# Optimization experiments

Hardware: AMD Instinct MI355X
Metric: run time of the kernel (lower is better)

The kernel has to match this reference:

```python
import jax, jax.numpy as jnp
import numpy as np

N, E, D = 100000, 1000000, 128  # nodes, edges, feature/embedding dim


def setup_inputs() -> dict:
    key = jax.random.key(0)
    ks = jax.random.split(key, 8)
    s = 1.0 / np.sqrt(D)
    return {
        "x": jax.random.normal(ks[0], (N, D), jnp.float32),
        "edge_index": jax.random.randint(ks[1], (2, E), 0, N, jnp.int32),
        # layer 1: lin_l (with bias) on aggregated neighbors, lin_r (no bias) on root
        "W1_l": jax.random.normal(ks[2], (D, D), jnp.float32) * s,
        "b1_l": jnp.zeros((D,), jnp.float32),
        "W1_r": jax.random.normal(ks[3], (D, D), jnp.float32) * s,
        # layer 2
        "W2_l": jax.random.normal(ks[4], (D, D), jnp.float32) * s,
        "b2_l": jnp.zeros((D,), jnp.float32),
        "W2_r": jax.random.normal(ks[5], (D, D), jnp.float32) * s,
    }


def _sage_conv(x, src, dst, Wl, bl, Wr):
    # PyG SAGEConv (aggr='mean'): out = lin_l(mean_{j->i} x_j) + lin_r(x_i)
    msgs = x[src]                                            # [E, D] gather
    agg = jax.ops.segment_sum(msgs, dst, num_segments=N)     # [N, D] scatter-add
    cnt = jax.ops.segment_sum(jnp.ones((src.shape[0],), x.dtype), dst,
                              num_segments=N)                # [N]
    mean = agg / jnp.maximum(cnt, 1.0)[:, None]
    return mean @ Wl + bl + x @ Wr


def reference(x, edge_index, W1_l, b1_l, W1_r, W2_l, b2_l, W2_r):
    src, dst = edge_index[0], edge_index[1]
    h = jax.nn.relu(_sage_conv(x, src, dst, W1_l, b1_l, W1_r))  # dropout inactive (eval)
    return _sage_conv(h, src, dst, W2_l, b2_l, W2_r)            # [N, D] embeddings
```

## Files before the change

kernel.cpp:

```cpp
#include <hip/hip_runtime.h>

#define D 128
constexpr int NPB   = 128;
constexpr int BCAP  = 1536;
constexpr int SEGB  = 8192;
constexpr int KMAX  = 1024;

typedef __bf16 bf16x8 __attribute__((ext_vector_type(8)));
typedef float f32x4 __attribute__((ext_vector_type(4)));
typedef int intv4 __attribute__((ext_vector_type(4)));

__device__ __forceinline__ unsigned short f2bf(float f) {
    unsigned int u = __float_as_uint(f);
    unsigned int r = (u + 0x7fffu + ((u >> 16) & 1u)) >> 16;
    return (unsigned short)r;
}
__device__ __forceinline__ unsigned pack2(float a, float b) {
    return (unsigned)f2bf(a) | ((unsigned)f2bf(b) << 16);
}
__device__ __forceinline__ int q8clamp(float v) {
    int q = __float2int_rn(v);
    return min(max(q, -127), 127);
}

__global__ __launch_bounds__(256) void front_kernel(
    const int* __restrict__ src, const int* __restrict__ dst,
    unsigned long long* __restrict__ bucket, int* __restrict__ bCur,
    int E, int K, int NB,
    const float* __restrict__ W1l, const float* __restrict__ W1r,
    const float* __restrict__ W2l, const float* __restrict__ W2r,
    unsigned short* __restrict__ Wpack,
    const float* __restrict__ xin, unsigned short* __restrict__ xb,
    unsigned* __restrict__ xq, float* __restrict__ sx, int n4)
{
    const int t = threadIdx.x;
    if (blockIdx.x < (unsigned)NB) {
        __shared__ int lcnt[KMAX], lbase[KMAX];
        for (int i = t; i < K; i += 256) lcnt[i] = 0;
        __syncthreads();

        const int base = blockIdx.x * SEGB;
        intv4 dreg[8], sreg[8];
#pragma unroll
        for (int c = 0; c < 4; ++c) {
            int e0 = base + c * 2048 + t * 8;
            if (e0 + 8 <= E) {
                dreg[2*c]   = __builtin_nontemporal_load(reinterpret_cast<const intv4*>(dst + e0));
                dreg[2*c+1] = __builtin_nontemporal_load(reinterpret_cast<const intv4*>(dst + e0 + 4));
                sreg[2*c]   = __builtin_nontemporal_load(reinterpret_cast<const intv4*>(src + e0));
                sreg[2*c+1] = __builtin_nontemporal_load(reinterpret_cast<const intv4*>(src + e0 + 4));
            } else {
#pragma unroll
                for (int k = 0; k < 4; ++k) {
                    dreg[2*c][k]   = (e0 + k < E) ? dst[e0 + k] : -1;
                    dreg[2*c+1][k] = (e0 + 4 + k < E) ? dst[e0 + 4 + k] : -1;
                    sreg[2*c][k]   = (e0 + k < E) ? src[e0 + k] : 0;
                    sreg[2*c+1][k] = (e0 + 4 + k < E) ? src[e0 + 4 + k] : 0;
                }
            }
#pragma unroll
            for (int k = 0; k < 8; ++k) {
                int d = dreg[2*c + (k >> 2)][k & 3];
                if (d >= 0) atomicAdd(&lcnt[d >> 7], 1);
            }
        }
        __syncthreads();
        for (int i = t; i < K; i += 256) {
            int c = lcnt[i];
            lbase[i] = c ? atomicAdd(&bCur[i], c) : 0;
            lcnt[i] = 0;
        }
        __syncthreads();
#pragma unroll
        for (int c = 0; c < 4; ++c) {
#pragma unroll
            for (int k = 0; k < 8; ++k) {
                int d = dreg[2*c + (k >> 2)][k & 3];
                int s = sreg[2*c + (k >> 2)][k & 3];
                if (d >= 0) {
                    int b = d >> 7;
                    int p = lbase[b] + atomicAdd(&lcnt[b], 1);
                    if (p < BCAP)
                        bucket[(size_t)b * BCAP + p] =
                            ((unsigned long long)(unsigned)s << 32) | (unsigned)d;
                }
            }
        }
    } else if (blockIdx.x < (unsigned)(NB + 32)) {
        int b = (blockIdx.x - NB) * 4 + (t >> 6);
        int l = t & 63;
        int layer = b >> 6, wsel = (b >> 5) & 1, kt = (b >> 3) & 3, ct = b & 7;
        const float* W = layer ? (wsel ? W2r : W2l) : (wsel ? W1r : W1l);
        int k0  = kt * 32 + (l >> 4) * 8;
        int col = ct * 16 + (l & 15);
        unsigned short tmp[8];
#pragma unroll
        for (int j = 0; j < 8; ++j) tmp[j] = f2bf(W[(k0 + j) * D + col]);
        size_t fbase = (((size_t)layer * 64 + wsel * 32 + kt * 8 + ct) * 64 + l) * 8;
        uint4 o;
        o.x = (unsigned)tmp[0] | ((unsigned)tmp[1] << 16);
        o.y = (unsigned)tmp[2] | ((unsigned)tmp[3] << 16);
        o.z = (unsigned)tmp[4] | ((unsigned)tmp[5] << 16);
        o.w = (unsigned)tmp[6] | ((unsigned)tmp[7] << 16);
        *reinterpret_cast<uint4*>(Wpack + fbase) = o;
    } else {
        int i = (blockIdx.x - NB - 32) * 256 + t;
        if (i < n4) {
            float4 v = reinterpret_cast<const float4*>(xin)[i];
            ushort4 o;
            o.x = f2bf(v.x); o.y = f2bf(v.y); o.z = f2bf(v.z); o.w = f2bf(v.w);
            reinterpret_cast<ushort4*>(xb)[i] = o;
            float am = fmaxf(fmaxf(fabsf(v.x), fabsf(v.y)),
                             fmaxf(fabsf(v.z), fabsf(v.w)));
#pragma unroll
            for (int off = 1; off < 32; off <<= 1)
                am = fmaxf(am, __shfl_xor(am, off, 32));
            am = fmaxf(am, 1e-20f);
            float inv = 127.0f / am;
            unsigned q = ((unsigned)(q8clamp(v.x * inv) & 0xff))
                       | ((unsigned)(q8clamp(v.y * inv) & 0xff) << 8)
                       | ((unsigned)(q8clamp(v.z * inv) & 0xff) << 16)
                       | ((unsigned)(q8clamp(v.w * inv) & 0xff) << 24);
            xq[i] = q;
            if ((t & 31) == 0) sx[i >> 5] = am / 127.0f;
        }
    }
}

__global__ __launch_bounds__(256) void csrbuild_kernel(
    const unsigned long long* __restrict__ bucket, const int* __restrict__ bCur,
    int2* __restrict__ offe, int* __restrict__ csr, int K, int N)
{
    __shared__ unsigned long long ebuf[BCAP];
    __shared__ int lhist[NPB], sc[NPB], lcur[NPB];
    __shared__ int red[256];
    const int t = threadIdx.x;
    const int b = blockIdx.x;

    int s = 0;
    for (int i = t; i < b; i += 256) s += bCur[i];
    red[t] = s;
    __syncthreads();
    for (int o = 128; o; o >>= 1) {
        if (t < o) red[t] += red[t + o];
        __syncthreads();
    }
    const int gbase = red[0];
    const int cnt = min(bCur[b], BCAP);

    if (t < NPB) lhist[t] = 0;
    __syncthreads();

    const unsigned long long* bp = bucket + (size_t)b * BCAP;
    for (int i = t; i < cnt; i += 256) {
        unsigned long long e = bp[i];
        ebuf[i] = e;
        atomicAdd(&lhist[(int)(e & 127ULL)], 1);
    }
    __syncthreads();

    if (t < NPB) sc[t] = lhist[t];
    __syncthreads();
    for (int o = 1; o < NPB; o <<= 1) {
        int y = 0;
        if (t < NPB && t >= o) y = sc[t - o];
        __syncthreads();
        if (t < NPB) sc[t] += y;
        __syncthreads();
    }
    if (t < NPB) {
        int node = b * NPB + t;
        int excl = sc[t] - lhist[t];
        lcur[t] = excl;
        if (node < N) offe[node] = make_int2(gbase + excl, gbase + sc[t]);
    }
    __syncthreads();

    for (int i = t; i < cnt; i += 256) {
        unsigned long long e = ebuf[i];
        int dl = (int)(e & 127ULL);
        int p = gbase + atomicAdd(&lcur[dl], 1);
        csr[p] = (int)(e >> 32);
    }
}

__device__ __forceinline__ void acc8(uint2 v, float sc, float* acc) {
#pragma unroll
    for (int w = 0; w < 2; ++w) {
        unsigned x = w ? v.y : v.x;
#pragma unroll
        for (int b = 0; b < 4; ++b) {
            int e = (int)((signed char)((x >> (8 * b)) & 0xffu));
            acc[4 * w + b] = fmaf((float)e, sc, acc[4 * w + b]);
        }
    }
}

__global__ __launch_bounds__(256) void gather8_i8(
    const uint2* __restrict__ q8, const float* __restrict__ scales,
    const int2* __restrict__ offe, const int* __restrict__ csr,
    unsigned short* __restrict__ mean, int N)
{
    int tid = blockIdx.x * 256 + threadIdx.x;
    int n   = tid >> 4;
    int q   = tid & 15;
    if (n >= N) return;
    int2 be = offe[n];
    int b = be.x, e = be.y;
    const uint2* fp = q8 + q;

    float acc[8];
#pragma unroll
    for (int i = 0; i < 8; ++i) acc[i] = 0.f;

    int j = b;
    for (; j + 3 < e; j += 4) {
        int s0 = __builtin_nontemporal_load(csr + j);
        int s1 = __builtin_nontemporal_load(csr + j + 1);
        int s2 = __builtin_nontemporal_load(csr + j + 2);
        int s3 = __builtin_nontemporal_load(csr + j + 3);
        uint2 v0 = fp[(size_t)s0 * 16];
        uint2 v1 = fp[(size_t)s1 * 16];
        uint2 v2 = fp[(size_t)s2 * 16];
        uint2 v3 = fp[(size_t)s3 * 16];
        float c0 = scales[s0];
        float c1 = scales[s1];
        float c2 = scales[s2];
        float c3 = scales[s3];
        acc8(v0, c0, acc);
        acc8(v1, c1, acc);
        acc8(v2, c2, acc);
        acc8(v3, c3, acc);
    }
    for (; j < e; ++j) {
        int s0 = csr[j];
        uint2 v0 = fp[(size_t)s0 * 16];
        acc8(v0, scales[s0], acc);
    }
    float invd = 1.0f / (float)max(e - b, 1);
#pragma unroll
    for (int i = 0; i < 8; ++i) acc[i] *= invd;
    uint4 o;
    o.x = pack2(acc[0], acc[1]);
    o.y = pack2(acc[2], acc[3]);
    o.z = pack2(acc[4], acc[5]);
    o.w = pack2(acc[6], acc[7]);
    *reinterpret_cast<uint4*>(mean + (size_t)n * D + q * 8) = o;
}

template <int RELU, int OUT_BF16, int QUANT>
__global__ __launch_bounds__(256, 2) void sage_mfma(
    const unsigned short* __restrict__ meanb,
    const unsigned short* __restrict__ xb,
    const unsigned short* __restrict__ Wpack,
    const float* __restrict__ bl,
    void* __restrict__ outv,
    signed char* __restrict__ hq, float* __restrict__ sh,
    int Mtiles, int TPB)
{
    __shared__ __align__(16) char sbuf[2][8192];
    __shared__ int rowmaxI[16];
    const int t    = threadIdx.x;
    const int lane = t & 63;
    const int wc   = t >> 6;
    const int l15  = lane & 15;
    const int lhi  = lane >> 4;

    bf16x8 bfrag[2][8];
#pragma unroll
    for (int ktt = 0; ktt < 8; ++ktt) {
        int wsel = ktt >> 2, kt = ktt & 3;
#pragma unroll
        for (int c = 0; c < 2; ++c) {
            int ct = wc * 2 + c;
            size_t fbase = ((size_t)(wsel * 32 + kt * 8 + ct) * 64 + lane) * 8;
            bfrag[c][ktt] = *reinterpret_cast<const bf16x8*>(Wpack + fbase);
        }
    }
    float bias[2];
    bias[0] = bl[wc * 32 + l15];
    bias[1] = bl[wc * 32 + 16 + l15];

    int tile0 = blockIdx.x * TPB;
    if (tile0 >= Mtiles) return;
    int tend = min(tile0 + TPB, Mtiles);

    const int sr = t >> 4;
    const int sq = t & 15;
    const int ss = sq ^ (sr & 7);
    char* dstM = &sbuf[0][sr * 256 + ss * 16];
    char* dstX = &sbuf[0][4096 + sr * 256 + ss * 16];

    {
        size_t gofs = (size_t)(tile0 * 16 + sr) * D + sq * 8;
        *reinterpret_cast<uint4*>(dstM) = *reinterpret_cast<const uint4*>(meanb + gofs);
        *reinterpret_cast<uint4*>(dstX) = *reinterpret_cast<const uint4*>(xb + gofs);
    }
    int cur = 0;

    for (int it = tile0; it < tend; ++it) {
        __syncthreads();
        const bool pf = (it + 1 < tend);
        uint4 mv, xv;
        if (pf) {
            size_t gofs = (size_t)((it + 1) * 16 + sr) * D + sq * 8;
            mv = *reinterpret_cast<const uint4*>(meanb + gofs);
            xv = *reinterpret_cast<const uint4*>(xb + gofs);
        }

        f32x4 acc0 = {0.f, 0.f, 0.f, 0.f};
        f32x4 acc1 = {0.f, 0.f, 0.f, 0.f};
        const char* base = sbuf[cur];
#pragma unroll
        for (int ktt = 0; ktt < 8; ++ktt) {
            int p = ktt >> 2, kt = ktt & 3;
            int q = kt * 4 + lhi;
            int byteoff = p * 4096 + l15 * 256 + ((q ^ (l15 & 7)) * 16);
            bf16x8 a = *reinterpret_cast<const bf16x8*>(base + byteoff);
            acc0 = __builtin_amdgcn_mfma_f32_16x16x32_bf16(a, bfrag[0][ktt], acc0, 0, 0, 0);
            acc1 = __builtin_amdgcn_mfma_f32_16x16x32_bf16(a, bfrag[1][ktt], acc1, 0, 0, 0);
        }

        int rbase = it * 16 + lhi * 4;
        float v[2][4];
#pragma unroll
        for (int c = 0; c < 2; ++c) {
            const f32x4& a = c ? acc1 : acc0;
#pragma unroll
            for (int r = 0; r < 4; ++r) {
                float w = a[r] + bias[c];
                if (RELU) w = fmaxf(w, 0.f);
                v[c][r] = w;
            }
        }
#pragma unroll
        for (int c = 0; c < 2; ++c) {
            int col = wc * 32 + c * 16 + l15;
#pragma unroll
            for (int r = 0; r < 4; ++r) {
                if (OUT_BF16) {
                    ((unsigned short*)outv)[(size_t)(rbase + r) * D + col] = f2bf(v[c][r]);
                } else {
                    ((float*)outv)[(size_t)(rbase + r) * D + col] = v[c][r];
                }
            }
        }

        if (QUANT) {
            float m[4];
#pragma unroll
            for (int r = 0; r < 4; ++r) m[r] = fmaxf(v[0][r], v[1][r]);
#pragma unroll
            for (int mask = 1; mask < 16; mask <<= 1)
#pragma unroll
                for (int r = 0; r < 4; ++r)
                    m[r] = fmaxf(m[r], __shfl_xor(m[r], mask, 64));
            __syncthreads();
            if (t < 16) rowmaxI[t] = 0;
            __syncthreads();
            if (l15 == 0) {
#pragma unroll
                for (int r = 0; r < 4; ++r)
                    atomicMax(&rowmaxI[lhi * 4 + r], __float_as_int(m[r]));
            }
            __syncthreads();
#pragma unroll
            for (int r = 0; r < 4; ++r) {
                float rm = __int_as_float(rowmaxI[lhi * 4 + r]);
                float inv = 127.0f / fmaxf(rm, 1e-20f);
                int row = rbase + r;
#pragma unroll
                for (int c = 0; c < 2; ++c) {
                    int col = wc * 32 + c * 16 + l15;
                    hq[(size_t)row * D + col] = (signed char)q8clamp(v[c][r] * inv);
                }
                if (wc == 0 && l15 == 0) sh[row] = rm / 127.0f;
            }
        }

        if (pf) {
            char* dM = dstM + (cur ^ 1) * 8192;
            char* dX = dstX + (cur ^ 1) * 8192;
            *reinterpret_cast<uint4*>(dM) = mv;
            *reinterpret_cast<uint4*>(dX) = xv;
            cur ^= 1;
        }
    }
}

extern "C" void kernel_launch(void* const* d_in, const int* in_sizes, int n_in,
                              void* d_out, int out_size, void* d_ws, size_t ws_size,
                              hipStream_t stream) {
    const float* x   = (const float*)d_in[0];
    const int*   ei  = (const int*)d_in[1];
    const float* W1l = (const float*)d_in[2];
    const float* b1l = (const float*)d_in[3];
    const float* W1r = (const float*)d_in[4];
    const float* W2l = (const float*)d_in[5];
    const float* b2l = (const float*)d_in[6];
    const float* W2r = (const float*)d_in[7];
    float* out = (float*)d_out;

    const int N = in_sizes[0] / D;
    const int E = in_sizes[1] / 2;
    const int* src = ei;
    const int* dst = ei + E;

    const int K = (N + NPB - 1) / NPB;

    unsigned short* xb    = (unsigned short*)d_ws;
    unsigned short* meanb = xb + (size_t)N * D;
    unsigned short* hb    = meanb + (size_t)N * D;
    unsigned short* Wpack = hb + (size_t)N * D;
    int* bCur     = (int*)(Wpack + 65536);
    int2* offe    = (int2*)(bCur + KMAX);
    int* csr_src  = (int*)(offe + N);
    float* sx     = (float*)(csr_src + E);
    float* sh     = sx + N;
    signed char* hq = (signed char*)(sh + N);

    unsigned long long* bucket = (unsigned long long*)hb;
    unsigned* xq = (unsigned*)((char*)hb + (size_t)K * BCAP * 8);

    const int Mtiles  = (N + 15) / 16;
    const int TPB     = 8;
    const int gemmGrid = (Mtiles + TPB - 1) / TPB;
    const int gatherBlocks = (int)(((long long)N * 16 + 255) / 256);
    const int NB = (E + SEGB - 1) / SEGB;
    const int n4 = N * D / 4;
    const int convBlocks = (n4 + 255) / 256;

    hipMemsetAsync(bCur, 0, (size_t)K * sizeof(int), stream);
    front_kernel<<<NB + 32 + convBlocks, 256, 0, stream>>>(
        src, dst, bucket, bCur, E, K, NB,
        W1l, W1r, W2l, W2r, Wpack, x, xb, xq, sx, n4);
    csrbuild_kernel<<<K, 256, 0, stream>>>(bucket, bCur, offe, csr_src, K, N);

    gather8_i8<<<gatherBlocks, 256, 0, stream>>>(
        (const uint2*)xq, sx, offe, csr_src, meanb, N);
    sage_mfma<1, 1, 1><<<gemmGrid, 256, 0, stream>>>(
        meanb, xb, Wpack, b1l, hb, hq, sh, Mtiles, TPB);

    gather8_i8<<<gatherBlocks, 256, 0, stream>>>(
        (const uint2*)hq, sh, offe, csr_src, meanb, N);
    sage_mfma<0, 0, 0><<<gemmGrid, 256, 0, stream>>>(
        meanb, hb, Wpack + 32768, b2l, out, nullptr, nullptr, Mtiles, TPB);
}
```

Before: 149.8 us.

## Fuse neighbor mean-gather into the MFMA SAGE layer kernel

Replaces the separate int8 gather kernel and the bf16 MFMA GEMM kernel with one kernel per layer. Each block gathers and averages neighbor features for its 16-row tile directly into LDS, then runs the MFMA GEMM on that tile. This removes the write and re-read of the intermediate mean buffer and one launch per layer. In exchange it drops the double-buffered prefetch, exposes gather latency between barriers, lowers tiles per block and adds a 3-blocks-per-CU launch bound that may limit occupancy for the latency-bound gather. The quantized input buffer is moved into the now-unused mean workspace so it does not overlap the hidden-layer output written in the same kernel.

```diff
diff --git a/kernel.cpp b/kernel.cpp
--- a/kernel.cpp
+++ b/kernel.cpp
@@ -196,69 +196,18 @@
     }
 }
 
-__global__ __launch_bounds__(256) void gather8_i8(
+template <int RELU, int OUT_BF16, int QUANT>
+__global__ __launch_bounds__(256, 3) void sage_fused(
     const uint2* __restrict__ q8, const float* __restrict__ scales,
     const int2* __restrict__ offe, const int* __restrict__ csr,
-    unsigned short* __restrict__ mean, int N)
-{
-    int tid = blockIdx.x * 256 + threadIdx.x;
-    int n   = tid >> 4;
-    int q   = tid & 15;
-    if (n >= N) return;
-    int2 be = offe[n];
-    int b = be.x, e = be.y;
-    const uint2* fp = q8 + q;
-
-    float acc[8];
-#pragma unroll
-    for (int i = 0; i < 8; ++i) acc[i] = 0.f;
-
-    int j = b;
-    for (; j + 3 < e; j += 4) {
-        int s0 = __builtin_nontemporal_load(csr + j);
-        int s1 = __builtin_nontemporal_load(csr + j + 1);
-        int s2 = __builtin_nontemporal_load(csr + j + 2);
-        int s3 = __builtin_nontemporal_load(csr + j + 3);
-        uint2 v0 = fp[(size_t)s0 * 16];
-        uint2 v1 = fp[(size_t)s1 * 16];
-        uint2 v2 = fp[(size_t)s2 * 16];
-        uint2 v3 = fp[(size_t)s3 * 16];
-        float c0 = scales[s0];
-        float c1 = scales[s1];
-        float c2 = scales[s2];
-        float c3 = scales[s3];
-        acc8(v0, c0, acc);
-        acc8(v1, c1, acc);
-        acc8(v2, c2, acc);
-        acc8(v3, c3, acc);
-    }
-    for (; j < e; ++j) {
-        int s0 = csr[j];
-        uint2 v0 = fp[(size_t)s0 * 16];
-        acc8(v0, scales[s0], acc);
-    }
-    float invd = 1.0f / (float)max(e - b, 1);
-#pragma unroll
-    for (int i = 0; i < 8; ++i) acc[i] *= invd;
-    uint4 o;
-    o.x = pack2(acc[0], acc[1]);
-    o.y = pack2(acc[2], acc[3]);
-    o.z = pack2(acc[4], acc[5]);
-    o.w = pack2(acc[6], acc[7]);
-    *reinterpret_cast<uint4*>(mean + (size_t)n * D + q * 8) = o;
-}
-
-template <int RELU, int OUT_BF16, int QUANT>
-__global__ __launch_bounds__(256, 2) void sage_mfma(
-    const unsigned short* __restrict__ meanb,
-    const unsigned short* __restrict__ xb,
+    const unsigned short* __restrict__ xside,
     const unsigned short* __restrict__ Wpack,
     const float* __restrict__ bl,
     void* __restrict__ outv,
     signed char* __restrict__ hq, float* __restrict__ sh,
-    int Mtiles, int TPB)
+    int Mtiles, int TPB, int N)
 {
-    __shared__ __align__(16) char sbuf[2][8192];
+    __shared__ __align__(16) char sbuf[8192];
     __shared__ int rowmaxI[16];
     const int t    = threadIdx.x;
     const int lane = t & 63;
@@ -288,35 +237,69 @@
     const int sr = t >> 4;
     const int sq = t & 15;
     const int ss = sq ^ (sr & 7);
-    char* dstM = &sbuf[0][sr * 256 + ss * 16];
-    char* dstX = &sbuf[0][4096 + sr * 256 + ss * 16];
-
-    {
-        size_t gofs = (size_t)(tile0 * 16 + sr) * D + sq * 8;
-        *reinterpret_cast<uint4*>(dstM) = *reinterpret_cast<const uint4*>(meanb + gofs);
-        *reinterpret_cast<uint4*>(dstX) = *reinterpret_cast<const uint4*>(xb + gofs);
-    }
-    int cur = 0;
+    char* dstM = &sbuf[sr * 256 + ss * 16];
+    char* dstX = &sbuf[4096 + sr * 256 + ss * 16];
+    const uint2* fp = q8 + sq;
 
     for (int it = tile0; it < tend; ++it) {
-        __syncthreads();
-        const bool pf = (it + 1 < tend);
-        uint4 mv, xv;
-        if (pf) {
-            size_t gofs = (size_t)((it + 1) * 16 + sr) * D + sq * 8;
-            mv = *reinterpret_cast<const uint4*>(meanb + gofs);
-            xv = *reinterpret_cast<const uint4*>(xb + gofs);
-        }
+        const int n = it * 16 + sr;
+
+        uint4 xv = make_uint4(0, 0, 0, 0);
+        if (n < N) xv = *reinterpret_cast<const uint4*>(xside + (size_t)n * D + sq * 8);
+
+        float acc[8];
+#pragma unroll
+        for (int i = 0; i < 8; ++i) acc[i] = 0.f;
+        if (n < N) {
+            int2 be = offe[n];
+            int jb = be.x, je = be.y;
+            int j = jb;
+            for (; j + 3 < je; j += 4) {
+                int s0 = __builtin_nontemporal_load(csr + j);
+                int s1 = __builtin_nontemporal_load(csr + j + 1);
+                int s2 = __builtin_nontemporal_load(csr + j + 2);
+                int s3 = __builtin_nontemporal_load(csr + j + 3);
+                uint2 v0 = fp[(size_t)s0 * 16];
+                uint2 v1 = fp[(size_t)s1 * 16];
+                uint2 v2 = fp[(size_t)s2 * 16];
+                uint2 v3 = fp[(size_t)s3 * 16];
+                float c0 = scales[s0];
+                float c1 = scales[s1];
+                float c2 = scales[s2];
+                float c3 = scales[s3];
+                acc8(v0, c0, acc);
+                acc8(v1, c1, acc);
+                acc8(v2, c2, acc);
+                acc8(v3, c3, acc);
+            }
+            for (; j < je; ++j) {
+                int s0 = csr[j];
+                uint2 v0 = fp[(size_t)s0 * 16];
+                acc8(v0, scales[s0], acc);
+            }
+            float invd = 1.0f / (float)max(je - jb, 1);
+#pragma unroll
+            for (int i = 0; i < 8; ++i) acc[i] *= invd;
+        }
+        uint4 mv;
+        mv.x = pack2(acc[0], acc[1]);
+        mv.y = pack2(acc[2], acc[3]);
+        mv.z = pack2(acc[4], acc[5]);
+        mv.w = pack2(acc[6], acc[7]);
+
+        __syncthreads();
+        *reinterpret_cast<uint4*>(dstM) = mv;
+        *reinterpret_cast<uint4*>(dstX) = xv;
+        __syncthreads();
 
         f32x4 acc0 = {0.f, 0.f, 0.f, 0.f};
         f32x4 acc1 = {0.f, 0.f, 0.f, 0.f};
-        const char* base = sbuf[cur];
 #pragma unroll
         for (int ktt = 0; ktt < 8; ++ktt) {
             int p = ktt >> 2, kt = ktt & 3;
             int q = kt * 4 + lhi;
             int byteoff = p * 4096 + l15 * 256 + ((q ^ (l15 & 7)) * 16);
-            bf16x8 a = *reinterpret_cast<const bf16x8*>(base + byteoff);
+            bf16x8 a = *reinterpret_cast<const bf16x8*>(sbuf + byteoff);
             acc0 = __builtin_amdgcn_mfma_f32_16x16x32_bf16(a, bfrag[0][ktt], acc0, 0, 0, 0);
             acc1 = __builtin_amdgcn_mfma_f32_16x16x32_bf16(a, bfrag[1][ktt], acc1, 0, 0, 0);
         }
@@ -338,10 +321,13 @@
             int col = wc * 32 + c * 16 + l15;
 #pragma unroll
             for (int r = 0; r < 4; ++r) {
-                if (OUT_BF16) {
-                    ((unsigned short*)outv)[(size_t)(rbase + r) * D + col] = f2bf(v[c][r]);
-                } else {
-                    ((float*)outv)[(size_t)(rbase + r) * D + col] = v[c][r];
+                int row = rbase + r;
+                if (row < N) {
+                    if (OUT_BF16) {
+                        ((unsigned short*)outv)[(size_t)row * D + col] = f2bf(v[c][r]);
+                    } else {
+                        ((float*)outv)[(size_t)row * D + col] = v[c][r];
+                    }
                 }
             }
         }
@@ -369,21 +355,15 @@
                 float rm = __int_as_float(rowmaxI[lhi * 4 + r]);
                 float inv = 127.0f / fmaxf(rm, 1e-20f);
                 int row = rbase + r;
-#pragma unroll
-                for (int c = 0; c < 2; ++c) {
-                    int col = wc * 32 + c * 16 + l15;
-                    hq[(size_t)row * D + col] = (signed char)q8clamp(v[c][r] * inv);
+                if (row < N) {
+#pragma unroll
+                    for (int c = 0; c < 2; ++c) {
+                        int col = wc * 32 + c * 16 + l15;
+                        hq[(size_t)row * D + col] = (signed char)q8clamp(v[c][r] * inv);
+                    }
+                    if (wc == 0 && l15 == 0) sh[row] = rm / 127.0f;
                 }
-                if (wc == 0 && l15 == 0) sh[row] = rm / 127.0f;
-            }
-        }
-
-        if (pf) {
-            char* dM = dstM + (cur ^ 1) * 8192;
-            char* dX = dstX + (cur ^ 1) * 8192;
-            *reinterpret_cast<uint4*>(dM) = mv;
-            *reinterpret_cast<uint4*>(dX) = xv;
-            cur ^= 1;
+            }
         }
     }
 }
@@ -420,12 +400,11 @@
     signed char* hq = (signed char*)(sh + N);
 
     unsigned long long* bucket = (unsigned long long*)hb;
-    unsigned* xq = (unsigned*)((char*)hb + (size_t)K * BCAP * 8);
+    unsigned* xq = (unsigned*)meanb;
 
     const int Mtiles  = (N + 15) / 16;
-    const int TPB     = 8;
-    const int gemmGrid = (Mtiles + TPB - 1) / TPB;
-    const int gatherBlocks = (int)(((long long)N * 16 + 255) / 256);
+    const int TPB     = 4;
+    const int fusedGrid = (Mtiles + TPB - 1) / TPB;
     const int NB = (E + SEGB - 1) / SEGB;
     const int n4 = N * D / 4;
     const int convBlocks = (n4 + 255) / 256;
@@ -436,13 +415,11 @@
         W1l, W1r, W2l, W2r, Wpack, x, xb, xq, sx, n4);
     csrbuild_kernel<<<K, 256, 0, stream>>>(bucket, bCur, offe, csr_src, K, N);
 
-    gather8_i8<<<gatherBlocks, 256, 0, stream>>>(
-        (const uint2*)xq, sx, offe, csr_src, meanb, N);
-    sage_mfma<1, 1, 1><<<gemmGrid, 256, 0, stream>>>(
-        meanb, xb, Wpack, b1l, hb, hq, sh, Mtiles, TPB);
-
-    gather8_i8<<<gatherBlocks, 256, 0, stream>>>(
-        (const uint2*)hq, sh, offe, csr_src, meanb, N);
-    sage_mfma<0, 0, 0><<<gemmGrid, 256, 0, stream>>>(
-        meanb, hb, Wpack + 32768, b2l, out, nullptr, nullptr, Mtiles, TPB);
-}
+    sage_fused<1, 1, 1><<<fusedGrid, 256, 0, stream>>>(
+        (const uint2*)xq, sx, offe, csr_src, xb, Wpack, b1l,
+        hb, hq, sh, Mtiles, TPB, N);
+
+    sage_fused<0, 0, 0><<<fusedGrid, 256, 0, stream>>>(
+        (const uint2*)hq, sh, offe, csr_src, hb, Wpack + 32768, b2l,
+        out, nullptr, nullptr, Mtiles, TPB, N);
+}
```

After: 205.3 us. 37.0% more time.

## Use int8-quantized root features in GEMMs and drop bf16 copies of x and h

Applied to the files above, without the earlier changes.

The GEMM kernels now read the root-node features from the int8 quantized buffers (xq/hq plus per-row scales) and dequantize them to bf16 while staging into shared memory, instead of reading separate bf16 copies. The bf16 conversion of x in the front kernel and the bf16 write of h in the first GEMM are removed. This cuts global memory traffic for writes and reads of N×D bf16 arrays. In exchange the root term carries int8 quantization error, adds dequantization ALU work, and the workspace layout is reorganized with row bounds checks added.

```diff
diff --git a/kernel.cpp b/kernel.cpp
--- a/kernel.cpp
+++ b/kernel.cpp
@@ -21,6 +21,20 @@
 __device__ __forceinline__ int q8clamp(float v) {
     int q = __float2int_rn(v);
     return min(max(q, -127), 127);
+}
+__device__ __forceinline__ uint4 deq8(uint2 v, float s) {
+    float f[8];
+#pragma unroll
+    for (int w = 0; w < 2; ++w) {
+        unsigned x = w ? v.y : v.x;
+#pragma unroll
+        for (int b = 0; b < 4; ++b)
+            f[4 * w + b] = (float)((int)(signed char)((x >> (8 * b)) & 0xffu)) * s;
+    }
+    uint4 o;
+    o.x = pack2(f[0], f[1]); o.y = pack2(f[2], f[3]);
+    o.z = pack2(f[4], f[5]); o.w = pack2(f[6], f[7]);
+    return o;
 }
 
 __global__ __launch_bounds__(256) void front_kernel(
@@ -30,7 +44,7 @@
     const float* __restrict__ W1l, const float* __restrict__ W1r,
     const float* __restrict__ W2l, const float* __restrict__ W2r,
     unsigned short* __restrict__ Wpack,
-    const float* __restrict__ xin, unsigned short* __restrict__ xb,
+    const float* __restrict__ xin,
     unsigned* __restrict__ xq, float* __restrict__ sx, int n4)
 {
     const int t = threadIdx.x;
@@ -107,9 +121,6 @@
         int i = (blockIdx.x - NB - 32) * 256 + t;
         if (i < n4) {
             float4 v = reinterpret_cast<const float4*>(xin)[i];
-            ushort4 o;
-            o.x = f2bf(v.x); o.y = f2bf(v.y); o.z = f2bf(v.z); o.w = f2bf(v.w);
-            reinterpret_cast<ushort4*>(xb)[i] = o;
             float am = fmaxf(fmaxf(fabsf(v.x), fabsf(v.y)),
                              fmaxf(fabsf(v.z), fabsf(v.w)));
 #pragma unroll
@@ -248,15 +259,15 @@
     *reinterpret_cast<uint4*>(mean + (size_t)n * D + q * 8) = o;
 }
 
-template <int RELU, int OUT_BF16, int QUANT>
+template <int RELU, int QUANT>
 __global__ __launch_bounds__(256, 2) void sage_mfma(
     const unsigned short* __restrict__ meanb,
-    const unsigned short* __restrict__ xb,
+    const uint2* __restrict__ xq8, const float* __restrict__ sxa,
     const unsigned short* __restrict__ Wpack,
     const float* __restrict__ bl,
-    void* __restrict__ outv,
+    float* __restrict__ outf,
     signed char* __restrict__ hq, float* __restrict__ sh,
-    int Mtiles, int TPB)
+    int Mtiles, int TPB, int N)
 {
     __shared__ __align__(16) char sbuf[2][8192];
     __shared__ int rowmaxI[16];
@@ -292,20 +303,26 @@
     char* dstX = &sbuf[0][4096 + sr * 256 + ss * 16];
 
     {
-        size_t gofs = (size_t)(tile0 * 16 + sr) * D + sq * 8;
+        int n = tile0 * 16 + sr;
+        size_t gofs = (size_t)n * D + sq * 8;
         *reinterpret_cast<uint4*>(dstM) = *reinterpret_cast<const uint4*>(meanb + gofs);
-        *reinterpret_cast<uint4*>(dstX) = *reinterpret_cast<const uint4*>(xb + gofs);
+        uint2 xv = xq8[(size_t)n * 16 + sq];
+        *reinterpret_cast<uint4*>(dstX) = deq8(xv, sxa[n]);
     }
     int cur = 0;
 
     for (int it = tile0; it < tend; ++it) {
         __syncthreads();
         const bool pf = (it + 1 < tend);
-        uint4 mv, xv;
+        uint4 mv;
+        uint2 xv;
+        float xs;
         if (pf) {
-            size_t gofs = (size_t)((it + 1) * 16 + sr) * D + sq * 8;
+            int n = (it + 1) * 16 + sr;
+            size_t gofs = (size_t)n * D + sq * 8;
             mv = *reinterpret_cast<const uint4*>(meanb + gofs);
-            xv = *reinterpret_cast<const uint4*>(xb + gofs);
+            xv = xq8[(size_t)n * 16 + sq];
+            xs = sxa[n];
         }
 
         f32x4 acc0 = {0.f, 0.f, 0.f, 0.f};
@@ -333,18 +350,6 @@
                 v[c][r] = w;
             }
         }
-#pragma unroll
-        for (int c = 0; c < 2; ++c) {
-            int col = wc * 32 + c * 16 + l15;
-#pragma unroll
-            for (int r = 0; r < 4; ++r) {
-                if (OUT_BF16) {
-                    ((unsigned short*)outv)[(size_t)(rbase + r) * D + col] = f2bf(v[c][r]);
-                } else {
-                    ((float*)outv)[(size_t)(rbase + r) * D + col] = v[c][r];
-                }
-            }
-        }
 
         if (QUANT) {
             float m[4];
@@ -369,12 +374,24 @@
                 float rm = __int_as_float(rowmaxI[lhi * 4 + r]);
                 float inv = 127.0f / fmaxf(rm, 1e-20f);
                 int row = rbase + r;
-#pragma unroll
-                for (int c = 0; c < 2; ++c) {
-                    int col = wc * 32 + c * 16 + l15;
-                    hq[(size_t)row * D + col] = (signed char)q8clamp(v[c][r] * inv);
+                if (row < N) {
+#pragma unroll
+                    for (int c = 0; c < 2; ++c) {
+                        int col = wc * 32 + c * 16 + l15;
+                        hq[(size_t)row * D + col] = (signed char)q8clamp(v[c][r] * inv);
+                    }
+                    if (wc == 0 && l15 == 0) sh[row] = rm / 127.0f;
                 }
-                if (wc == 0 && l15 == 0) sh[row] = rm / 127.0f;
+            }
+        } else {
+#pragma unroll
+            for (int c = 0; c < 2; ++c) {
+                int col = wc * 32 + c * 16 + l15;
+#pragma unroll
+                for (int r = 0; r < 4; ++r) {
+                    int row = rbase + r;
+                    if (row < N) outf[(size_t)row * D + col] = v[c][r];
+                }
             }
         }
 
@@ -382,7 +399,7 @@
             char* dM = dstM + (cur ^ 1) * 8192;
             char* dX = dstX + (cur ^ 1) * 8192;
             *reinterpret_cast<uint4*>(dM) = mv;
-            *reinterpret_cast<uint4*>(dX) = xv;
+            *reinterpret_cast<uint4*>(dX) = deq8(xv, xs);
             cur ^= 1;
         }
     }
@@ -408,19 +425,16 @@
 
     const int K = (N + NPB - 1) / NPB;
 
-    unsigned short* xb    = (unsigned short*)d_ws;
-    unsigned short* meanb = xb + (size_t)N * D;
-    unsigned short* hb    = meanb + (size_t)N * D;
-    unsigned short* Wpack = hb + (size_t)N * D;
+    unsigned long long* bucket = (unsigned long long*)d_ws;
+    unsigned short* meanb = (unsigned short*)(bucket + (size_t)KMAX * BCAP);
+    unsigned* xq   = (unsigned*)(meanb + (size_t)N * D);
+    signed char* hq = (signed char*)((char*)xq + (size_t)N * D);
+    unsigned short* Wpack = (unsigned short*)(hq + (size_t)N * D);
     int* bCur     = (int*)(Wpack + 65536);
     int2* offe    = (int2*)(bCur + KMAX);
     int* csr_src  = (int*)(offe + N);
     float* sx     = (float*)(csr_src + E);
     float* sh     = sx + N;
-    signed char* hq = (signed char*)(sh + N);
-
-    unsigned long long* bucket = (unsigned long long*)hb;
-    unsigned* xq = (unsigned*)((char*)hb + (size_t)K * BCAP * 8);
 
     const int Mtiles  = (N + 15) / 16;
     const int TPB     = 8;
@@ -433,16 +447,16 @@
     hipMemsetAsync(bCur, 0, (size_t)K * sizeof(int), stream);
     front_kernel<<<NB + 32 + convBlocks, 256, 0, stream>>>(
         src, dst, bucket, bCur, E, K, NB,
-        W1l, W1r, W2l, W2r, Wpack, x, xb, xq, sx, n4);
+        W1l, W1r, W2l, W2r, Wpack, x, xq, sx, n4);
     csrbuild_kernel<<<K, 256, 0, stream>>>(bucket, bCur, offe, csr_src, K, N);
 
     gather8_i8<<<gatherBlocks, 256, 0, stream>>>(
         (const uint2*)xq, sx, offe, csr_src, meanb, N);
-    sage_mfma<1, 1, 1><<<gemmGrid, 256, 0, stream>>>(
-        meanb, xb, Wpack, b1l, hb, hq, sh, Mtiles, TPB);
+    sage_mfma<1, 1><<<gemmGrid, 256, 0, stream>>>(
+        meanb, (const uint2*)xq, sx, Wpack, b1l, nullptr, hq, sh, Mtiles, TPB, N);
 
     gather8_i8<<<gatherBlocks, 256, 0, stream>>>(
         (const uint2*)hq, sh, offe, csr_src, meanb, N);
-    sage_mfma<0, 0, 0><<<gemmGrid, 256, 0, stream>>>(
-        meanb, hb, Wpack + 32768, b2l, out, nullptr, nullptr, Mtiles, TPB);
-}
+    sage_mfma<0, 0><<<gemmGrid, 256, 0, stream>>>(
+        meanb, (const uint2*)hq, sh, Wpack + 32768, b2l, out, nullptr, nullptr, Mtiles, TPB, N);
+}
```

Measured after the change: 145.0 us. 3.2% less time.
